# Kernel optimization log

Hardware: AMD Instinct MI355X
Metric: run time of the kernel (lower is better)

## Reference

```python
import jax, jax.numpy as jnp
import numpy as np

B, H, S, D = 2, 8, 2048, 64
WINDOW = 3            # local_attention_window (default in torch forward)
FRAC = 0.3            # percentage_frac hardcoded in create_window_tensor call
MASK_FILL = -1.0e9


def window_kernel(window, frac):
    # create_window_tensor: [ (1-f)^n ... (1-f)^1, 1, (1-f)^1 ... (1-f)^n ]
    n = (window - 1) // 2
    side = np.array([(1.0 - frac) ** i for i in range(n, 0, -1)], dtype=np.float32)
    vals = np.concatenate([side, np.array([1.0], np.float32), side[::-1]])
    return jnp.asarray(vals)


def setup_inputs() -> dict:
    key = jax.random.key(0)
    kq, kk, kv = jax.random.split(key, 3)
    queries = jax.random.normal(kq, (B, H, S, D), jnp.float32)
    keys = jax.random.normal(kk, (B, H, S, D), jnp.float32)
    values = jax.random.normal(kv, (B, H, S, D), jnp.float32)
    # causal mask: True positions are filled with -1e9 (masked_fill semantics)
    mask = jnp.triu(jnp.ones((S, S), dtype=bool), 1)[None, None]  # [1,1,S,S]
    # linear_bias: nn.Parameter(torch.zeros(Sk)) created inside forward
    beta = jnp.zeros((S,), jnp.float32)
    return {"queries": queries, "keys": keys, "values": values,
            "beta": beta, "mask": mask}


def reference(queries, keys, values, beta, mask):
    d = keys.shape[-1]
    # scores = Q K^T / sqrt(d)
    scores = jnp.einsum("bhqd,bhkd->bhqk", queries, keys) / jnp.sqrt(
        jnp.asarray(d, queries.dtype))
    scores = jnp.where(mask, jnp.asarray(MASK_FILL, scores.dtype), scores)
    # include_local_attention=True, local_attention_dim_vertical=False:
    # the torch code transposes, conv2d with a [1,W] kernel along the last
    # axis, transposes back -> 1D cross-correlation along the QUERY axis.
    # Kernel is symmetric so correlation == convolution. Zero padding.
    kern = window_kernel(WINDOW, FRAC)
    p = (WINDOW - 1) // 2
    xp = jnp.pad(scores, ((0, 0), (0, 0), (p, p), (0, 0)))
    Sq = scores.shape[2]
    scores = sum(kern[i] * jax.lax.dynamic_slice_in_dim(xp, i, Sq, axis=2)
                 for i in range(WINDOW))
    # linear_bias=True: add zero-initialized per-key-position bias
    scores = scores + beta  # broadcasts over last dim [Sk]
    weights = jax.nn.softmax(scores, axis=-1)
    return jnp.einsum("bhqk,bhkd->bhqd", weights, values)
```

## Files before the change

kernel.cpp:

```cpp
#include <hip/hip_runtime.h>


typedef short bf16x8 __attribute__((ext_vector_type(8)));
typedef float f32x4  __attribute__((ext_vector_type(4)));

constexpr int S_ = 2048;
constexpr int D_ = 64;
constexpr float LOG2E = 1.44269504088896341f;
constexpr float KSC = 0.125f * LOG2E;

__device__ __forceinline__ unsigned pk2(float lo, float hi) {
    union { float f; unsigned u; } a, b;
    a.f = lo; b.f = hi;
    return __builtin_amdgcn_perm(b.u + 0x8000u, a.u + 0x8000u, 0x07060302u);
}

__global__ __launch_bounds__(256)
void cvt8(const float* __restrict__ K, const float* __restrict__ V,
          unsigned short* __restrict__ F)
{
    __shared__ float T[64][68];

    const int bid = blockIdx.x;
    const int hd = bid & 15, tt = bid >> 4;
    const float* Kt = K + ((size_t)hd * S_ + tt * 64) * D_;
    const float* Vt = V + ((size_t)hd * S_ + tt * 64) * D_;
    unsigned short* Ft = F + (size_t)(hd * 32 + tt) * 8192;

    const int t = threadIdx.x;
    const int key = t >> 2, d0 = (t & 3) << 4;

    {
        const float* vp = Vt + key * D_ + d0;
        #pragma unroll
        for (int i = 0; i < 4; ++i) {
            float4 v4 = *(const float4*)(vp + 4 * i);
            T[d0 + 4 * i + 0][key] = v4.x;
            T[d0 + 4 * i + 1][key] = v4.y;
            T[d0 + 4 * i + 2][key] = v4.z;
            T[d0 + 4 * i + 3][key] = v4.w;
        }
    }

    {
        const float* kp = Kt + key * D_ + d0;
        float4 a = *(const float4*)(kp);
        float4 b = *(const float4*)(kp + 4);
        float4 c = *(const float4*)(kp + 8);
        float4 d = *(const float4*)(kp + 12);
        uint4 w0 = make_uint4(pk2(a.x, a.y), pk2(a.z, a.w), pk2(b.x, b.y), pk2(b.z, b.w));
        uint4 w1 = make_uint4(pk2(c.x, c.y), pk2(c.z, c.w), pk2(d.x, d.y), pk2(d.z, d.w));
        const int r5 = key & 31;
        const int kh = key >> 5, mb = (r5 >> 2) & 1;
        const int n = ((r5 >> 3) << 2) | (r5 & 3);
        const int hh = d0 >> 5, qd0 = (d0 >> 3) & 3;
        const int f0 = (kh << 2) | (mb << 1) | hh;
        *(uint4*)(Ft + f0 * 512 + ((qd0 << 4) | n) * 8)       = w0;
        *(uint4*)(Ft + f0 * 512 + (((qd0 + 1) << 4) | n) * 8) = w1;
    }
    __syncthreads();

    #pragma unroll
    for (int s = 0; s < 2; ++s) {
        const int slot = t + s * 256;
        const int fr = slot >> 6, lane = slot & 63;
        const int kh = fr >> 2, mb = fr & 3, n = lane & 15, qd = lane >> 4;
        const float* row = &T[mb * 16 + n][kh * 32 + qd * 8];
        uint4 w = make_uint4(pk2(row[0], row[1]), pk2(row[2], row[3]),
                             pk2(row[4], row[5]), pk2(row[6], row[7]));
        *(uint4*)(Ft + (8 + fr) * 512 + lane * 8) = w;
    }
}

#define LD_KA(TILE, KA) do {                                                 \
    const unsigned short* fq_ = Fh + (size_t)(TILE) * 8192;                  \
    KA[0][0] = *(const bf16x8*)(fq_ + kfo[0][0]);                            \
    KA[0][1] = *(const bf16x8*)(fq_ + kfo[0][1]);                            \
    KA[1][0] = *(const bf16x8*)(fq_ + kfo[1][0]);                            \
    KA[1][1] = *(const bf16x8*)(fq_ + kfo[1][1]);                            \
} while (0)

#define COMP_T(TILE, KA, PRE) do {                                           \
    const int kb_ = ((TILE) << 6) + kvo;                                     \
    const unsigned short* fp_ = Fh + (size_t)(TILE) * 8192;                  \
    const bf16x8 vb0_ = *(const bf16x8*)(fp_ + vfo[0]);                      \
    const bf16x8 vb1_ = *(const bf16x8*)(fp_ + vfo[1]);                      \
    const bf16x8 vb2_ = *(const bf16x8*)(fp_ + vfo[2]);                      \
    const bf16x8 vb3_ = *(const bf16x8*)(fp_ + vfo[3]);                      \
    const float4 b0_ = *(const float4*)&bl[kb_];                             \
    const float4 b1_ = *(const float4*)&bl[kb_ + 4];                         \
    const float bt_[8] = {b0_.x, b0_.y, b0_.z, b0_.w,                        \
                          b1_.x, b1_.y, b1_.z, b1_.w};                       \
    const f32x4 zz_ = {0, 0, 0, 0};                                          \
    f32x4 acc_[2][2];                                                        \
    acc_[0][0] = __builtin_amdgcn_mfma_f32_16x16x32_bf16(KA[0][1], qb[0][1], \
        __builtin_amdgcn_mfma_f32_16x16x32_bf16(KA[0][0], qb[0][0], zz_, 0, 0, 0), 0, 0, 0); \
    acc_[0][1] = __builtin_amdgcn_mfma_f32_16x16x32_bf16(KA[0][1], qb[1][1], \
        __builtin_amdgcn_mfma_f32_16x16x32_bf16(KA[0][0], qb[1][0], zz_, 0, 0, 0), 0, 0, 0); \
    acc_[1][0] = __builtin_amdgcn_mfma_f32_16x16x32_bf16(KA[1][1], qb[0][1], \
        __builtin_amdgcn_mfma_f32_16x16x32_bf16(KA[1][0], qb[0][0], zz_, 0, 0, 0), 0, 0, 0); \
    acc_[1][1] = __builtin_amdgcn_mfma_f32_16x16x32_bf16(KA[1][1], qb[1][1], \
        __builtin_amdgcn_mfma_f32_16x16x32_bf16(KA[1][0], qb[1][0], zz_, 0, 0, 0), 0, 0, 0); \
    PRE;                                                                     \
    const bool dm_ = (TILE) == nt - 1;                                       \
    _Pragma("unroll")                                                        \
    for (int ng_ = 0; ng_ < 2; ++ng_) {                                      \
        const int qr_ = qbase + (ng_ << 4) + n_l;                            \
        float pv_[8];                                                        \
        float la_ = 0.0f;                                                    \
        _Pragma("unroll")                                                    \
        for (int jj_ = 0; jj_ < 8; ++jj_) {                                  \
            float sv_ = fmaf(acc_[jj_ >> 2][ng_][jj_ & 3], KSC, bt_[jj_]);   \
            if (dm_) {                                                       \
                const int key_ = kb_ + jj_;                                  \
                if (!((key_ < qr_) || (qr_ == 0 && key_ == 0))) sv_ = -1.0e30f; \
            }                                                                \
            pv_[jj_] = __builtin_amdgcn_exp2f(sv_);                          \
            la_ += pv_[jj_];                                                 \
        }                                                                    \
        l[ng_] += la_;                                                       \
        union { unsigned u[4]; bf16x8 v; } pf_;                              \
        pf_.u[0] = pk2(pv_[0], pv_[1]);                                      \
        pf_.u[1] = pk2(pv_[2], pv_[3]);                                      \
        pf_.u[2] = pk2(pv_[4], pv_[5]);                                      \
        pf_.u[3] = pk2(pv_[6], pv_[7]);                                      \
        o[0][ng_] = __builtin_amdgcn_mfma_f32_16x16x32_bf16(vb0_, pf_.v, o[0][ng_], 0, 0, 0); \
        o[1][ng_] = __builtin_amdgcn_mfma_f32_16x16x32_bf16(vb1_, pf_.v, o[1][ng_], 0, 0, 0); \
        o[2][ng_] = __builtin_amdgcn_mfma_f32_16x16x32_bf16(vb2_, pf_.v, o[2][ng_], 0, 0, 0); \
        o[3][ng_] = __builtin_amdgcn_mfma_f32_16x16x32_bf16(vb3_, pf_.v, o[3][ng_], 0, 0, 0); \
    }                                                                        \
} while (0)

__global__ __launch_bounds__(512, 4)
void attn17(const float* __restrict__ Q, const float* __restrict__ beta,
            const unsigned short* __restrict__ F, float* __restrict__ out)
{
    __shared__ float slab[2][64][72];
    __shared__ float bl[S_];

    const int bid = blockIdx.x;
    const int hd = bid & 15;
    const int rest = bid >> 4;
    const int j = (rest < 16) ? (31 - 2 * rest) : (2 * (rest - 16));

    const int q0 = j << 6;
    const int nt = j + 1;

    const float* Qh = Q + (size_t)hd * S_ * D_;
    const unsigned short* Fh = F + (size_t)hd * 32 * 8192;

    const int t = threadIdx.x, lane = t & 63;
    const int wv = t >> 6;
    const int kh = wv & 1, par = (wv >> 1) & 1, qh = wv >> 2;
    const int n_l = lane & 15, qd = lane >> 4;
    const int qbase = q0 + (qh << 5);

    #pragma unroll
    for (int i = 0; i < 4; ++i) bl[t + i * 512] = beta[t + i * 512] * LOG2E;
    __syncthreads();

    const int lo = lane * 8;
    int kfo[2][2], vfo[4];
    #pragma unroll
    for (int mb = 0; mb < 2; ++mb)
        #pragma unroll
        for (int hh = 0; hh < 2; ++hh)
            kfo[mb][hh] = ((kh << 2) | (mb << 1) | hh) * 512 + lo;
    #pragma unroll
    for (int mb = 0; mb < 4; ++mb)
        vfo[mb] = (8 + (kh << 2) + mb) * 512 + lo;

    const int kvo = (kh << 5) + (qd << 3);

    bf16x8 qb[2][2];
    #pragma unroll
    for (int ng = 0; ng < 2; ++ng) {
        const int q = qbase + (ng << 4) + n_l;
        const float wp = (q > 0) ? 0.7f : 0.0f;
        const float wn = (q + 1 < S_) ? 0.7f : 0.0f;
        const float* qc = Qh + (size_t)q * D_;
        const float* qpp = qc - ((q > 0) ? D_ : 0);
        const float* qnn = qc + ((q + 1 < S_) ? D_ : 0);
        #pragma unroll
        for (int hh = 0; hh < 2; ++hh) {
            const int d0 = (hh << 5) + (qd << 3);
            float4 c0 = *(const float4*)(qc + d0),  c1 = *(const float4*)(qc + d0 + 4);
            float4 p0 = *(const float4*)(qpp + d0), p1 = *(const float4*)(qpp + d0 + 4);
            float4 n0 = *(const float4*)(qnn + d0), n1 = *(const float4*)(qnn + d0 + 4);
            float e0 = fmaf(wn, n0.x, fmaf(wp, p0.x, c0.x));
            float e1 = fmaf(wn, n0.y, fmaf(wp, p0.y, c0.y));
            float e2 = fmaf(wn, n0.z, fmaf(wp, p0.z, c0.z));
            float e3 = fmaf(wn, n0.w, fmaf(wp, p0.w, c0.w));
            float e4 = fmaf(wn, n1.x, fmaf(wp, p1.x, c1.x));
            float e5 = fmaf(wn, n1.y, fmaf(wp, p1.y, c1.y));
            float e6 = fmaf(wn, n1.z, fmaf(wp, p1.z, c1.z));
            float e7 = fmaf(wn, n1.w, fmaf(wp, p1.w, c1.w));
            union { unsigned u[4]; bf16x8 v; } qu;
            qu.u[0] = pk2(e0, e1); qu.u[1] = pk2(e2, e3);
            qu.u[2] = pk2(e4, e5); qu.u[3] = pk2(e6, e7);
            qb[ng][hh] = qu.v;
        }
    }

    f32x4 o[4][2];
    float l[2] = {0.0f, 0.0f};
    #pragma unroll
    for (int mb = 0; mb < 4; ++mb)
        #pragma unroll
        for (int ng = 0; ng < 2; ++ng) o[mb][ng] = (f32x4){0, 0, 0, 0};

    bf16x8 ka[2][2];
    int it = par;
    if (it < nt) {
        LD_KA(it, ka);
        for (; it + 2 < nt; it += 2) {
            COMP_T(it, ka, LD_KA(it + 2, ka));
        }
        COMP_T(it, ka, (void)0);
    }

    #pragma unroll
    for (int ng = 0; ng < 2; ++ng) {
        l[ng] += __shfl_xor(l[ng], 16);
        l[ng] += __shfl_xor(l[ng], 32);
    }
    if (par == 1) {
        #pragma unroll
        for (int ng = 0; ng < 2; ++ng) {
            const int row = (qh << 5) + (ng << 4) + n_l;
            #pragma unroll
            for (int mb = 0; mb < 4; ++mb)
                *(float4*)&slab[kh][row][(mb << 4) + (qd << 2)] =
                    make_float4(o[mb][ng][0], o[mb][ng][1], o[mb][ng][2], o[mb][ng][3]);
            if (qd == 0) slab[kh][row][64] = l[ng];
        }
    }
    __syncthreads();
    if (par == 0) {
        #pragma unroll
        for (int ng = 0; ng < 2; ++ng) {
            const int row = (qh << 5) + (ng << 4) + n_l;
            #pragma unroll
            for (int mb = 0; mb < 4; ++mb) {
                float4 pv4 = *(float4*)&slab[kh][row][(mb << 4) + (qd << 2)];
                o[mb][ng][0] += pv4.x; o[mb][ng][1] += pv4.y;
                o[mb][ng][2] += pv4.z; o[mb][ng][3] += pv4.w;
            }
            l[ng] += slab[kh][row][64];
            if (kh == 0) {
                #pragma unroll
                for (int mb = 0; mb < 4; ++mb)
                    *(float4*)&slab[0][row][(mb << 4) + (qd << 2)] =
                        make_float4(o[mb][ng][0], o[mb][ng][1], o[mb][ng][2], o[mb][ng][3]);
                if (qd == 0) slab[0][row][64] = l[ng];
            }
        }
    }
    __syncthreads();
    if (par == 0 && kh == 1) {
        #pragma unroll
        for (int ng = 0; ng < 2; ++ng) {
            const int row = (qh << 5) + (ng << 4) + n_l;
            const float inv = 1.0f / (l[ng] + slab[0][row][64]);
            float* op = out + ((size_t)hd * S_ + q0 + row) * D_ + (qd << 2);
            #pragma unroll
            for (int mb = 0; mb < 4; ++mb) {
                float4 pv4 = *(float4*)&slab[0][row][(mb << 4) + (qd << 2)];
                *(float4*)(op + (mb << 4)) =
                    make_float4((o[mb][ng][0] + pv4.x) * inv, (o[mb][ng][1] + pv4.y) * inv,
                                (o[mb][ng][2] + pv4.z) * inv, (o[mb][ng][3] + pv4.w) * inv);
            }
        }
    }
}

#undef LD_KA
#undef COMP_T

extern "C" void kernel_launch(void* const* d_in, const int* in_sizes, int n_in,
                              void* d_out, int out_size, void* d_ws, size_t ws_size,
                              hipStream_t stream) {
    const float* Q    = (const float*)d_in[0];
    const float* K    = (const float*)d_in[1];
    const float* V    = (const float*)d_in[2];
    const float* beta = (const float*)d_in[3];
    float* out = (float*)d_out;

    unsigned short* F = (unsigned short*)d_ws;

    cvt8<<<dim3(512), 256, 0, stream>>>(K, V, F);
    attn17<<<dim3(512), 512, 0, stream>>>(Q, beta, F, out);
}
```

Measured before the change: 115.3 us.

## Stage K/V fragments through LDS with four-slot prefetch pipeline

Replaces direct per-wave global loads of the packed K/V fragments with a cooperative block-wide copy into a four-slot LDS ring. The next two tiles are prefetched into registers while the current pair is computed, then stored, with one barrier per step. The wave-to-role mapping is also reshuffled, and the output-combine slab reuses the staging buffer. The aim is to cut redundant global/L2 traffic, since every wave used to fetch the same tile itself. In exchange it adds LDS capacity (launch bounds drop from 4 to 2 blocks per SM), a barrier per step, and LDS bandwidth pressure.

New measurement: 129.8 us. 12.6% more time.

```diff
diff --git a/kernel.cpp b/kernel.cpp
--- a/kernel.cpp
+++ b/kernel.cpp
@@ -72,36 +72,43 @@
     }
 }
 
-#define LD_KA(TILE, KA) do {                                                 \
-    const unsigned short* fq_ = Fh + (size_t)(TILE) * 8192;                  \
-    KA[0][0] = *(const bf16x8*)(fq_ + kfo[0][0]);                            \
-    KA[0][1] = *(const bf16x8*)(fq_ + kfo[0][1]);                            \
-    KA[1][0] = *(const bf16x8*)(fq_ + kfo[1][0]);                            \
-    KA[1][1] = *(const bf16x8*)(fq_ + kfo[1][1]);                            \
+#define STAGE_LD(TILE, A_, B_) do {                                          \
+    const unsigned short* gs_ = Fh + (size_t)(TILE) * 8192 + (t << 3);       \
+    A_ = *(const uint4*)gs_;                                                 \
+    B_ = *(const uint4*)(gs_ + 4096);                                        \
 } while (0)
 
-#define COMP_T(TILE, KA, PRE) do {                                           \
+#define STAGE_ST(TILE, A_, B_) do {                                          \
+    unsigned short* db_ = &fbuf[(TILE) & 3][t << 3];                         \
+    *(uint4*)db_ = A_;                                                       \
+    *(uint4*)(db_ + 4096) = B_;                                              \
+} while (0)
+
+#define COMP_T(TILE, FB) do {                                                \
+    const unsigned short* fb_ = (FB);                                        \
+    bf16x8 ka00_ = *(const bf16x8*)(fb_ + kfo[0][0]);                        \
+    bf16x8 ka01_ = *(const bf16x8*)(fb_ + kfo[0][1]);                        \
+    bf16x8 ka10_ = *(const bf16x8*)(fb_ + kfo[1][0]);                        \
+    bf16x8 ka11_ = *(const bf16x8*)(fb_ + kfo[1][1]);                        \
     const int kb_ = ((TILE) << 6) + kvo;                                     \
-    const unsigned short* fp_ = Fh + (size_t)(TILE) * 8192;                  \
-    const bf16x8 vb0_ = *(const bf16x8*)(fp_ + vfo[0]);                      \
-    const bf16x8 vb1_ = *(const bf16x8*)(fp_ + vfo[1]);                      \
-    const bf16x8 vb2_ = *(const bf16x8*)(fp_ + vfo[2]);                      \
-    const bf16x8 vb3_ = *(const bf16x8*)(fp_ + vfo[3]);                      \
     const float4 b0_ = *(const float4*)&bl[kb_];                             \
     const float4 b1_ = *(const float4*)&bl[kb_ + 4];                         \
     const float bt_[8] = {b0_.x, b0_.y, b0_.z, b0_.w,                        \
                           b1_.x, b1_.y, b1_.z, b1_.w};                       \
     const f32x4 zz_ = {0, 0, 0, 0};                                          \
     f32x4 acc_[2][2];                                                        \
-    acc_[0][0] = __builtin_amdgcn_mfma_f32_16x16x32_bf16(KA[0][1], qb[0][1], \
-        __builtin_amdgcn_mfma_f32_16x16x32_bf16(KA[0][0], qb[0][0], zz_, 0, 0, 0), 0, 0, 0); \
-    acc_[0][1] = __builtin_amdgcn_mfma_f32_16x16x32_bf16(KA[0][1], qb[1][1], \
-        __builtin_amdgcn_mfma_f32_16x16x32_bf16(KA[0][0], qb[1][0], zz_, 0, 0, 0), 0, 0, 0); \
-    acc_[1][0] = __builtin_amdgcn_mfma_f32_16x16x32_bf16(KA[1][1], qb[0][1], \
-        __builtin_amdgcn_mfma_f32_16x16x32_bf16(KA[1][0], qb[0][0], zz_, 0, 0, 0), 0, 0, 0); \
-    acc_[1][1] = __builtin_amdgcn_mfma_f32_16x16x32_bf16(KA[1][1], qb[1][1], \
-        __builtin_amdgcn_mfma_f32_16x16x32_bf16(KA[1][0], qb[1][0], zz_, 0, 0, 0), 0, 0, 0); \
-    PRE;                                                                     \
+    acc_[0][0] = __builtin_amdgcn_mfma_f32_16x16x32_bf16(ka01_, qb[0][1],    \
+        __builtin_amdgcn_mfma_f32_16x16x32_bf16(ka00_, qb[0][0], zz_, 0, 0, 0), 0, 0, 0); \
+    acc_[0][1] = __builtin_amdgcn_mfma_f32_16x16x32_bf16(ka01_, qb[1][1],    \
+        __builtin_amdgcn_mfma_f32_16x16x32_bf16(ka00_, qb[1][0], zz_, 0, 0, 0), 0, 0, 0); \
+    acc_[1][0] = __builtin_amdgcn_mfma_f32_16x16x32_bf16(ka11_, qb[0][1],    \
+        __builtin_amdgcn_mfma_f32_16x16x32_bf16(ka10_, qb[0][0], zz_, 0, 0, 0), 0, 0, 0); \
+    acc_[1][1] = __builtin_amdgcn_mfma_f32_16x16x32_bf16(ka11_, qb[1][1],    \
+        __builtin_amdgcn_mfma_f32_16x16x32_bf16(ka10_, qb[1][0], zz_, 0, 0, 0), 0, 0, 0); \
+    bf16x8 vb0_ = *(const bf16x8*)(fb_ + vfo[0]);                            \
+    bf16x8 vb1_ = *(const bf16x8*)(fb_ + vfo[1]);                            \
+    bf16x8 vb2_ = *(const bf16x8*)(fb_ + vfo[2]);                            \
+    bf16x8 vb3_ = *(const bf16x8*)(fb_ + vfo[3]);                            \
     const bool dm_ = (TILE) == nt - 1;                                       \
     _Pragma("unroll")                                                        \
     for (int ng_ = 0; ng_ < 2; ++ng_) {                                      \
@@ -131,12 +138,13 @@
     }                                                                        \
 } while (0)
 
-__global__ __launch_bounds__(512, 4)
-void attn17(const float* __restrict__ Q, const float* __restrict__ beta,
+__global__ __launch_bounds__(512, 2)
+void attn22(const float* __restrict__ Q, const float* __restrict__ beta,
             const unsigned short* __restrict__ F, float* __restrict__ out)
 {
-    __shared__ float slab[2][64][72];
+    __shared__ __align__(16) unsigned short fbuf[4][8192];
     __shared__ float bl[S_];
+    float* slabf = (float*)&fbuf[0][0];
 
     const int bid = blockIdx.x;
     const int hd = bid & 15;
@@ -151,13 +159,12 @@
 
     const int t = threadIdx.x, lane = t & 63;
     const int wv = t >> 6;
-    const int kh = wv & 1, par = (wv >> 1) & 1, qh = wv >> 2;
+    const int kh = wv & 1, qh = (wv >> 1) & 1, par = wv >> 2;
     const int n_l = lane & 15, qd = lane >> 4;
     const int qbase = q0 + (qh << 5);
 
     #pragma unroll
     for (int i = 0; i < 4; ++i) bl[t + i * 512] = beta[t + i * 512] * LOG2E;
-    __syncthreads();
 
     const int lo = lane * 8;
     int kfo[2][2], vfo[4];
@@ -209,14 +216,27 @@
         #pragma unroll
         for (int ng = 0; ng < 2; ++ng) o[mb][ng] = (f32x4){0, 0, 0, 0};
 
-    bf16x8 ka[2][2];
-    int it = par;
-    if (it < nt) {
-        LD_KA(it, ka);
-        for (; it + 2 < nt; it += 2) {
-            COMP_T(it, ka, LD_KA(it + 2, ka));
-        }
-        COMP_T(it, ka, (void)0);
+    {
+        uint4 a0, b0;
+        STAGE_LD(0, a0, b0);
+        STAGE_ST(0, a0, b0);
+        if (nt > 1) {
+            STAGE_LD(1, a0, b0);
+            STAGE_ST(1, a0, b0);
+        }
+    }
+    __syncthreads();
+
+    for (int base = 0; base < nt; base += 2) {
+        uint4 a2, b2, a3, b3;
+        const bool h2 = (base + 2 < nt), h3 = (base + 3 < nt);
+        if (h2) STAGE_LD(base + 2, a2, b2);
+        if (h3) STAGE_LD(base + 3, a3, b3);
+        const int myt = base + par;
+        if (myt < nt) COMP_T(myt, fbuf[myt & 3]);
+        if (h2) STAGE_ST(base + 2, a2, b2);
+        if (h3) STAGE_ST(base + 3, a3, b3);
+        __syncthreads();
     }
 
     #pragma unroll
@@ -230,9 +250,9 @@
             const int row = (qh << 5) + (ng << 4) + n_l;
             #pragma unroll
             for (int mb = 0; mb < 4; ++mb)
-                *(float4*)&slab[kh][row][(mb << 4) + (qd << 2)] =
+                *(float4*)&slabf[(kh * 64 + row) * 68 + (mb << 4) + (qd << 2)] =
                     make_float4(o[mb][ng][0], o[mb][ng][1], o[mb][ng][2], o[mb][ng][3]);
-            if (qd == 0) slab[kh][row][64] = l[ng];
+            if (qd == 0) slabf[(kh * 64 + row) * 68 + 64] = l[ng];
         }
     }
     __syncthreads();
@@ -242,17 +262,17 @@
             const int row = (qh << 5) + (ng << 4) + n_l;
             #pragma unroll
             for (int mb = 0; mb < 4; ++mb) {
-                float4 pv4 = *(float4*)&slab[kh][row][(mb << 4) + (qd << 2)];
+                float4 pv4 = *(float4*)&slabf[(kh * 64 + row) * 68 + (mb << 4) + (qd << 2)];
                 o[mb][ng][0] += pv4.x; o[mb][ng][1] += pv4.y;
                 o[mb][ng][2] += pv4.z; o[mb][ng][3] += pv4.w;
             }
-            l[ng] += slab[kh][row][64];
+            l[ng] += slabf[(kh * 64 + row) * 68 + 64];
             if (kh == 0) {
                 #pragma unroll
                 for (int mb = 0; mb < 4; ++mb)
-                    *(float4*)&slab[0][row][(mb << 4) + (qd << 2)] =
+                    *(float4*)&slabf[row * 68 + (mb << 4) + (qd << 2)] =
                         make_float4(o[mb][ng][0], o[mb][ng][1], o[mb][ng][2], o[mb][ng][3]);
-                if (qd == 0) slab[0][row][64] = l[ng];
+                if (qd == 0) slabf[row * 68 + 64] = l[ng];
             }
         }
     }
@@ -261,11 +281,11 @@
         #pragma unroll
         for (int ng = 0; ng < 2; ++ng) {
             const int row = (qh << 5) + (ng << 4) + n_l;
-            const float inv = 1.0f / (l[ng] + slab[0][row][64]);
+            const float inv = 1.0f / (l[ng] + slabf[row * 68 + 64]);
             float* op = out + ((size_t)hd * S_ + q0 + row) * D_ + (qd << 2);
             #pragma unroll
             for (int mb = 0; mb < 4; ++mb) {
-                float4 pv4 = *(float4*)&slab[0][row][(mb << 4) + (qd << 2)];
+                float4 pv4 = *(float4*)&slabf[row * 68 + (mb << 4) + (qd << 2)];
                 *(float4*)(op + (mb << 4)) =
                     make_float4((o[mb][ng][0] + pv4.x) * inv, (o[mb][ng][1] + pv4.y) * inv,
                                 (o[mb][ng][2] + pv4.z) * inv, (o[mb][ng][3] + pv4.w) * inv);
@@ -273,9 +293,6 @@
         }
     }
 }
-
-#undef LD_KA
-#undef COMP_T
 
 extern "C" void kernel_launch(void* const* d_in, const int* in_sizes, int n_in,
                               void* d_out, int out_size, void* d_ws, size_t ws_size,
@@ -289,5 +306,5 @@
     unsigned short* F = (unsigned short*)d_ws;
 
     cvt8<<<dim3(512), 256, 0, stream>>>(K, V, F);
-    attn17<<<dim3(512), 512, 0, stream>>>(Q, beta, F, out);
+    attn22<<<dim3(512), 512, 0, stream>>>(Q, beta, F, out);
 }
```
